# Kernel optimization log

Hardware: AMD Instinct MI355X
Metric: run time of the kernel (lower is better)

Reference implementation:

```python
import jax, jax.numpy as jnp
import numpy as np

B, S, N, M = 64, 512, 512, 128   # batch, sensory_size, state_size, motor_size
UNFOLDS = 6
DT = 0.1  # elapsed_time


def _gate(v, mu, sigma):
    # piecewise-linear 'sigmoid': clip((v - mu + sigma) / (2 sigma), 0, 1)
    # v: [B, P] -> [B, P, 1] broadcast against [P, N]
    return jnp.clip((v[..., None] - mu + sigma) / (2.0 * sigma), 0.0, 1.0)


def setup_inputs() -> dict:
    key = jax.random.key(0)
    ks = jax.random.split(key, 12)
    u = lambda k, sh, lo, hi: jax.random.uniform(k, sh, jnp.float32, lo, hi)
    inputs = jax.random.normal(ks[0], (B, S), dtype=jnp.float32)
    states = jax.random.normal(ks[1], (B, N), dtype=jnp.float32) * 0.1
    # parameters per _init_ranges
    tau = u(ks[2], (N,), 0.001, 2.0)
    b = u(ks[3], (N,), -0.2, 0.2)
    erev = jnp.where(jax.random.bernoulli(ks[4], 0.8, (N, N)), 1.0, -1.0).astype(jnp.float32)
    w = u(ks[5], (N, N), 0.001, 1.0)
    sigma = jnp.full((N, N), 0.5, jnp.float32)
    mu = jnp.full((N, N), 0.5, jnp.float32)
    sensory_erev = jnp.where(jax.random.bernoulli(ks[6], 0.8, (S, N)), 1.0, -1.0).astype(jnp.float32)
    sensory_w = u(ks[7], (S, N), 0.001, 1.0)
    sensory_sigma = jnp.full((S, N), 0.5, jnp.float32)
    sensory_mu = jnp.full((S, N), 0.5, jnp.float32)
    sparsity_mask = jax.random.bernoulli(ks[8], 0.3, (N, N)).astype(jnp.float32)
    sensory_sparsity_mask = jax.random.bernoulli(ks[9], 0.3, (S, N)).astype(jnp.float32)
    input_w = jnp.ones((S,), jnp.float32)
    input_b = jnp.zeros((S,), jnp.float32)
    output_w = jnp.ones((M,), jnp.float32)
    output_b = jnp.zeros((M,), jnp.float32)
    return dict(inputs=inputs, states=states, tau=tau, b=b, erev=erev, w=w,
                sigma=sigma, mu=mu, sensory_erev=sensory_erev, sensory_w=sensory_w,
                sensory_sigma=sensory_sigma, sensory_mu=sensory_mu,
                sparsity_mask=sparsity_mask, sensory_sparsity_mask=sensory_sparsity_mask,
                input_w=input_w, input_b=input_b, output_w=output_w, output_b=output_b)


def reference(inputs, states, tau, b, erev, w, sigma, mu,
              sensory_erev, sensory_w, sensory_sigma, sensory_mu,
              sparsity_mask, sensory_sparsity_mask,
              input_w, input_b, output_w, output_b):
    # input mapping (affine)
    x = inputs * input_w + input_b                                   # [B, S]
    # sensory synapses, computed once
    sa = _gate(x, sensory_mu, sensory_sigma) * sensory_sparsity_mask  # [B, S, N]
    s_rev = jnp.einsum('bsn,sn->bn', sa, sensory_erev)               # [B, N]
    s_w = jnp.einsum('bsn,sn->bn', sa, sensory_w)                    # [B, N]
    delta = DT / UNFOLDS

    def step(v, _):
        g = _gate(v, mu, sigma) * sparsity_mask                      # [B, N, N]
        sum_rev = jnp.einsum('bij,ij->bj', g, erev) + s_rev + b      # sum over presynaptic i
        sum_w = jnp.einsum('bij,ij->bj', g, w) + s_w
        k = 1.0 / (1.0 + sum_w)
        taun = tau * k
        q = taun / (taun + delta)
        v_new = q * v + (1.0 - q) * k * sum_rev
        return v_new, None

    v, _ = jax.lax.scan(step, states, None, length=UNFOLDS)
    # output mapping: slice last M neurons (M < N), then affine
    out = v[:, -M:] * output_w + output_b                            # [B, M]
    return out, v
```

## Files before the change

### kernel.cpp

```cpp
#include <hip/hip_runtime.h>
#include <string.h>

constexpr int cB = 64, cS = 512, cN = 512, cM = 128, cUNF = 6;
constexpr float cDELTA = 0.016666666666666666f;

constexpr int JT   = 16;
constexpr int NCB  = cN / JT;
constexpr int NBLK = 256;
constexpr int NT   = 1024;
constexpr int NCW  = 4;
constexpr int SLOT_STRIDE = 16;

constexpr size_t OFF_V0   = 0;
constexpr size_t OFF_V1   = (size_t)cB * cN;
constexpr size_t OFF_H0   = OFF_V1 + (size_t)cB * cN;
constexpr size_t OFF_H1   = OFF_H0 + (size_t)cB * cN / 2;
constexpr size_t OFF_SLOT = OFF_H1 + (size_t)cB * cN / 2;
constexpr size_t OFF_DONE = OFF_SLOT + 512;
constexpr size_t OFF_BAD  = OFF_DONE + 4096;
constexpr size_t OFF_PK   = 131072;
static_assert(OFF_BAD + 64 <= OFF_PK, "control region must not alias packed table");

typedef _Float16 half8 __attribute__((ext_vector_type(8)));
typedef float    floatx4 __attribute__((ext_vector_type(4)));

__device__ __forceinline__ float clamp01(float x) {
    return __builtin_amdgcn_fmed3f(x, 0.0f, 1.0f);
}

__device__ __forceinline__ unsigned pack2h(float lo, float hi) {
    _Float16 l = (_Float16)lo, h = (_Float16)hi;
    unsigned short ls, hs;
    memcpy(&ls, &l, 2); memcpy(&hs, &h, 2);
    return (unsigned)ls | ((unsigned)hs << 16);
}

__global__ __launch_bounds__(NT, 1)
void k_fused(const float* __restrict__ inputs, const float* __restrict__ states,
             const float* __restrict__ tau,    const float* __restrict__ bias,
             const float* __restrict__ erev,   const float* __restrict__ wgt,
             const float* __restrict__ sigma,  const float* __restrict__ mu,
             const float* __restrict__ serev,  const float* __restrict__ swgt,
             const float* __restrict__ ssigma, const float* __restrict__ smu,
             const float* __restrict__ mask,   const float* __restrict__ smask,
             const float* __restrict__ inw,    const float* __restrict__ inb,
             const float* __restrict__ outw,   const float* __restrict__ outb,
             float* __restrict__ out, float* __restrict__ ws)
{
    float* v0 = ws + OFF_V0;
    float* v1 = ws + OFF_V1;
    _Float16* h0 = (_Float16*)(ws + OFF_H0);
    _Float16* h1 = (_Float16*)(ws + OFF_H1);
    int* slots = (int*)(ws + OFF_SLOT);
    int* done  = (int*)(ws + OFF_DONE);
    int* badf  = (int*)(ws + OFF_BAD);
    unsigned* pk = (unsigned*)(ws + OFF_PK);

    const int tid = threadIdx.x, blk = blockIdx.x;

    {
        const unsigned g = (unsigned)blk * NT + tid;
        const int lr  = g & 15;
        const int qp  = (g >> 4) & 3;
        const int lg2 = (g >> 6) & 3;
        const int kk2 = (g >> 8) & 15;
        const int jt2 = (g >> 12) & 31;
        const int m2  = (g >> 17) & 1;

        const float* E  = m2 ? serev  : erev;
        const float* W  = m2 ? swgt   : wgt;
        const float* SG = m2 ? ssigma : sigma;
        const float* MU = m2 ? smu    : mu;
        const float* MK = m2 ? smask  : mask;

        const int j  = jt2 * JT + lr;
        const int i0 = kk2 * 32 + lg2 * 8 + qp * 2;
        const size_t o0 = (size_t)i0 * cN + j, o1 = o0 + cN;
        const float e0 = E[o0],  e1 = E[o1];
        const float w0 = W[o0],  w1 = W[o1];
        const float m0 = MK[o0], m1 = MK[o1];
        const float s0 = SG[o0], s1 = SG[o1];
        const float u0 = MU[o0], u1 = MU[o1];
        const bool bad = (m0 != 0.f && (s0 != 0.5f || u0 != 0.5f)) ||
                         (m1 != 0.f && (s1 != 0.5f || u1 != 0.5f));

        const unsigned ed = pack2h(e0 * m0, e1 * m1);
        const unsigned wd = pack2h(w0 * m0, w1 * m1);
        const int frag = kk2 * 64 + lg2 * 16 + lr;
        unsigned* base = pk + (size_t)jt2 * 16384 + (m2 * 2) * 4096 + frag * 4 + qp;
        __hip_atomic_store(base,        ed, __ATOMIC_RELAXED, __HIP_MEMORY_SCOPE_AGENT);
        __hip_atomic_store(base + 4096, wd, __ATOMIC_RELAXED, __HIP_MEMORY_SCOPE_AGENT);
        if (bad)
            __hip_atomic_store(&badf[m2 * 32 + jt2], 1,
                               __ATOMIC_RELAXED, __HIP_MEMORY_SCOPE_AGENT);
    }
    __syncthreads();
    if (tid == 0)
        __hip_atomic_store(&done[blk * SLOT_STRIDE], 1,
                           __ATOMIC_RELAXED, __HIP_MEMORY_SCOPE_AGENT);
    if (blk >= NCB) return;

    const int j0   = blk * JT;
    const int lane = tid & 63;
    const int wv   = tid >> 6;
    const int mt   = wv;
    const int lr   = lane & 15;
    const int lg   = lane >> 4;
    const int bj   = j0 + lr;
    const int arow = mt * 16 + lr;
    const int kbase = lg * 8;
    const int cb0  = mt * 16 + lg * 4;

    int* mySlot = slots + blk * SLOT_STRIDE;

    __shared__ _Float16 Hlds[32768];
    __shared__ int sAny;
    const half8* hfr = (const half8*)Hlds;

    if (tid == 0) sAny = 0;

    float vold[4] = {0.f, 0.f, 0.f, 0.f};
    float tau_j = 0.f, bias_j = 0.f, ow = 0.f, ob = 0.f;
    if (wv < NCW) {
#pragma unroll
        for (int r = 0; r < 4; ++r)
            vold[r] = states[(size_t)(cb0 + r) * cN + bj];
        tau_j  = tau[bj];
        bias_j = bias[bj];
        if (bj >= cN - cM) { ow = outw[bj - (cN - cM)]; ob = outb[bj - (cN - cM)]; }
    }

    if (tid < NBLK) {
        const int* sl = done + tid * SLOT_STRIDE;
        while (__hip_atomic_load(sl, __ATOMIC_RELAXED, __HIP_MEMORY_SCOPE_AGENT) < 1)
            __builtin_amdgcn_s_sleep(1);
    }
    __syncthreads();

    const bool fastR = (__hip_atomic_load(&badf[blk], __ATOMIC_RELAXED,
                                          __HIP_MEMORY_SCOPE_AGENT) != 1);
    const bool fastS = (__hip_atomic_load(&badf[32 + blk], __ATOMIC_RELAXED,
                                          __HIP_MEMORY_SCOPE_AGENT) != 1);
    if (tid < 32 &&
        __hip_atomic_load(&badf[tid], __ATOMIC_RELAXED,
                          __HIP_MEMORY_SCOPE_AGENT) == 1)
        sAny = 1;

    {
        const uint4* src = (const uint4*)pk + (size_t)blk * 4096;
        floatx4 tmp[4];
#pragma unroll
        for (int r = 0; r < 4; ++r)
            asm volatile("global_load_dwordx4 %0, %1, off sc0 sc1"
                         : "=v"(tmp[r]) : "v"(src + r * 1024 + tid) : "memory");
        asm volatile("s_waitcnt vmcnt(0)" ::: "memory");
        __builtin_amdgcn_sched_barrier(0);
#pragma unroll
        for (int r = 0; r < 4; ++r)
            ((uint4*)Hlds)[r * 1024 + tid] = __builtin_bit_cast(uint4, tmp[r]);
    }
    __syncthreads();
    const bool pubF32 = (sAny == 1);

    float srb[4] = {0.f, 0.f, 0.f, 0.f}, swv[4] = {0.f, 0.f, 0.f, 0.f};
    if (wv < NCW) {
        if (fastS) {
            floatx4 aR = {0.f, 0.f, 0.f, 0.f}, aW = {0.f, 0.f, 0.f, 0.f};
#pragma unroll
            for (int kk = 0; kk < 16; ++kk) {
                const int off = kk * 32 + kbase;
                const float4 xa = *(const float4*)(inputs + (size_t)arow * cS + off);
                const float4 xb = *(const float4*)(inputs + (size_t)arow * cS + off + 4);
                const float4 wa = *(const float4*)(inw + off);
                const float4 wb = *(const float4*)(inw + off + 4);
                const float4 ba = *(const float4*)(inb + off);
                const float4 bb = *(const float4*)(inb + off + 4);
                half8 ax;
                ax[0] = (_Float16)clamp01(fmaf(xa.x, wa.x, ba.x));
                ax[1] = (_Float16)clamp01(fmaf(xa.y, wa.y, ba.y));
                ax[2] = (_Float16)clamp01(fmaf(xa.z, wa.z, ba.z));
                ax[3] = (_Float16)clamp01(fmaf(xa.w, wa.w, ba.w));
                ax[4] = (_Float16)clamp01(fmaf(xb.x, wb.x, bb.x));
                ax[5] = (_Float16)clamp01(fmaf(xb.y, wb.y, bb.y));
                ax[6] = (_Float16)clamp01(fmaf(xb.z, wb.z, bb.z));
                ax[7] = (_Float16)clamp01(fmaf(xb.w, wb.w, bb.w));
                aR = __builtin_amdgcn_mfma_f32_16x16x32_f16(ax, hfr[2048 + kk * 64 + lane], aR, 0, 0, 0);
                aW = __builtin_amdgcn_mfma_f32_16x16x32_f16(ax, hfr[3072 + kk * 64 + lane], aW, 0, 0, 0);
            }
#pragma unroll
            for (int r = 0; r < 4; ++r) { srb[r] = aR[r] + bias_j; swv[r] = aW[r]; }
        } else {
            float sr4[4] = {0,0,0,0}, sw4[4] = {0,0,0,0};
            for (int s = 0; s < cS; ++s) {
                size_t o = (size_t)s * cN + bj;
                float mk = smask[o];
                float sg = ssigma[o];
                float a  = 0.5f / sg;
                float c  = fmaf(-smu[o], a, 0.5f);
                float ee = serev[o] * mk, ww = swgt[o] * mk;
                float iw = inw[s], ib = inb[s];
#pragma unroll
                for (int r = 0; r < 4; ++r) {
                    float x = fmaf(inputs[(size_t)(cb0 + r) * cS + s], iw, ib);
                    float g = clamp01(fmaf(x, a, c));
                    sr4[r] = fmaf(g, ee, sr4[r]);
                    sw4[r] = fmaf(g, ww, sw4[r]);
                }
            }
#pragma unroll
            for (int r = 0; r < 4; ++r) { srb[r] = sr4[r] + bias_j; swv[r] = sw4[r]; }
        }
    }

    for (int u = 0; u < cUNF; ++u) {
        const float*    vRp = (u == 0) ? states : ((u & 1) ? v0 : v1);
        const _Float16* hRp = (u & 1) ? h0 : h1;

        float sumE[4], sumW[4];
        if (wv < NCW) {
            if (fastR) {
                floatx4 aE = {0.f, 0.f, 0.f, 0.f}, aWc = {0.f, 0.f, 0.f, 0.f};
                if (u == 0) {
                    const float* vrow = states + (size_t)arow * cN + kbase;
#pragma unroll
                    for (int kk = 0; kk < 16; ++kk) {
                        const float4 va = *(const float4*)(vrow + kk * 32);
                        const float4 vb = *(const float4*)(vrow + kk * 32 + 4);
                        half8 a8;
                        a8[0] = (_Float16)clamp01(va.x);
                        a8[1] = (_Float16)clamp01(va.y);
                        a8[2] = (_Float16)clamp01(va.z);
                        a8[3] = (_Float16)clamp01(va.w);
                        a8[4] = (_Float16)clamp01(vb.x);
                        a8[5] = (_Float16)clamp01(vb.y);
                        a8[6] = (_Float16)clamp01(vb.z);
                        a8[7] = (_Float16)clamp01(vb.w);
                        aE  = __builtin_amdgcn_mfma_f32_16x16x32_f16(a8, hfr[kk * 64 + lane], aE,  0, 0, 0);
                        aWc = __builtin_amdgcn_mfma_f32_16x16x32_f16(a8, hfr[1024 + kk * 64 + lane], aWc, 0, 0, 0);
                    }
                } else {
                    floatx4 raw[16];
                    const _Float16* hrow = hRp + (size_t)arow * cN + kbase;
#pragma unroll
                    for (int kk = 0; kk < 16; ++kk)
                        asm volatile("global_load_dwordx4 %0, %1, off offset:%2 sc0 sc1"
                                     : "=v"(raw[kk]) : "v"(hrow), "n"(kk * 64) : "memory");
                    asm volatile("s_waitcnt vmcnt(0)" ::: "memory");
                    __builtin_amdgcn_sched_barrier(0);
#pragma unroll
                    for (int kk = 0; kk < 16; ++kk) {
                        const half8 a8 = __builtin_bit_cast(half8, raw[kk]);
                        aE  = __builtin_amdgcn_mfma_f32_16x16x32_f16(a8, hfr[kk * 64 + lane], aE,  0, 0, 0);
                        aWc = __builtin_amdgcn_mfma_f32_16x16x32_f16(a8, hfr[1024 + kk * 64 + lane], aWc, 0, 0, 0);
                    }
                }
#pragma unroll
                for (int r = 0; r < 4; ++r) { sumE[r] = aE[r]; sumW[r] = aWc[r]; }
            } else {
                float r4[4] = {0,0,0,0}, w4[4] = {0,0,0,0};
                for (int i = 0; i < cN; ++i) {
                    size_t o = (size_t)i * cN + bj;
                    float mk = mask[o];
                    float sg = sigma[o];
                    float a  = 0.5f / sg;
                    float c  = fmaf(-mu[o], a, 0.5f);
                    float ee = erev[o] * mk, ww = wgt[o] * mk;
#pragma unroll
                    for (int r = 0; r < 4; ++r) {
                        float vi = __hip_atomic_load(&vRp[(size_t)(cb0 + r) * cN + i],
                                                     __ATOMIC_RELAXED, __HIP_MEMORY_SCOPE_AGENT);
                        float g = clamp01(fmaf(vi, a, c));
                        r4[r] = fmaf(g, ee, r4[r]);
                        w4[r] = fmaf(g, ww, w4[r]);
                    }
                }
#pragma unroll
                for (int r = 0; r < 4; ++r) { sumE[r] = r4[r]; sumW[r] = w4[r]; }
            }

#pragma unroll
            for (int r = 0; r < 4; ++r) {
                float rr   = sumE[r] + srb[r];
                float wsum = sumW[r] + swv[r];
                float k    = 1.0f / (1.0f + wsum);
                float taun = tau_j * k;
                float inv  = 1.0f / (taun + cDELTA);
                float vn   = (taun * inv) * vold[r] + (cDELTA * inv) * k * rr;
                vold[r] = vn;
            }
        }

        if (u < cUNF - 1) {
            if (wv < NCW) {
                float*    vWp = (u & 1) ? v1 : v0;
                _Float16* hWp = (u & 1) ? h1 : h0;
#pragma unroll
                for (int r = 0; r < 4; ++r) {
                    if (pubF32)
                        __hip_atomic_store(&vWp[(size_t)(cb0 + r) * cN + bj], vold[r],
                                           __ATOMIC_RELAXED, __HIP_MEMORY_SCOPE_AGENT);
                    _Float16 g = (_Float16)clamp01(vold[r]);
                    unsigned short gs;
                    memcpy(&gs, &g, 2);
                    unsigned int gi = gs;
                    asm volatile("global_store_short %0, %1, off sc0 sc1"
                                 :: "v"(hWp + (size_t)(cb0 + r) * cN + bj), "v"(gi)
                                 : "memory");
                }
            }
            __syncthreads();
            if (tid == 0)
                __hip_atomic_store(mySlot, u + 1,
                                   __ATOMIC_RELAXED, __HIP_MEMORY_SCOPE_AGENT);
            if (wv < NCW) {
                const int* sl = slots + (lane & 31) * SLOT_STRIDE;
                bool ok;
                do {
                    int v = (lane < 32)
                        ? __hip_atomic_load(sl, __ATOMIC_RELAXED, __HIP_MEMORY_SCOPE_AGENT)
                        : 0x7fffffff;
                    ok = __all((int)(v >= u + 1));
                } while (!ok);
            }
        }
    }

    if (wv < NCW) {
        float* vout = out + (size_t)cB * cM;
#pragma unroll
        for (int r = 0; r < 4; ++r) {
            int b = cb0 + r;
            vout[(size_t)b * cN + bj] = vold[r];
            if (bj >= cN - cM)
                out[(size_t)b * cM + (bj - (cN - cM))] = fmaf(vold[r], ow, ob);
        }
    }
}

extern "C" void kernel_launch(void* const* d_in, const int* in_sizes, int n_in,
                              void* d_out, int out_size, void* d_ws, size_t ws_size,
                              hipStream_t stream)
{
    const float* inputs = (const float*)d_in[0];
    const float* states = (const float*)d_in[1];
    const float* tau    = (const float*)d_in[2];
    const float* bias   = (const float*)d_in[3];
    const float* erev   = (const float*)d_in[4];
    const float* wgt    = (const float*)d_in[5];
    const float* sigma  = (const float*)d_in[6];
    const float* mu     = (const float*)d_in[7];
    const float* serev  = (const float*)d_in[8];
    const float* swgt   = (const float*)d_in[9];
    const float* ssigma = (const float*)d_in[10];
    const float* smu    = (const float*)d_in[11];
    const float* mask   = (const float*)d_in[12];
    const float* smask  = (const float*)d_in[13];
    const float* inw    = (const float*)d_in[14];
    const float* inb    = (const float*)d_in[15];
    const float* outw   = (const float*)d_in[16];
    const float* outb   = (const float*)d_in[17];
    float* out = (float*)d_out;
    float* ws  = (float*)d_ws;

    k_fused<<<NBLK, NT, 0, stream>>>(inputs, states, tau, bias, erev, wgt,
                                     sigma, mu, serev, swgt, ssigma, smu,
                                     mask, smask, inw, inb, outw, outb,
                                     out, ws);
}
```

Measured before the change: 131.0 us.

## Precompute fp16 gated inputs and initial states in the packing phase

The prologue threads of the persistent kernel (grid index 196608 and up) now also compute the clamped affine input gate and the clamped initial states, store them as packed fp16 in new workspace buffers, and the compute blocks read these with plain vector loads. This takes the per-element fp32 loads, FMAs, clamps and conversions off the serial critical path of the 32 compute blocks. The change also swaps the inline-asm cache-bypassing load of the packed table for ordinary loads, which depend on the done-flag barrier for visibility, and adds a short sleep in the inter-block spin-wait. The workspace layout is moved to fixed offsets to fit the new buffers.

```diff
diff --git a/kernel.cpp b/kernel.cpp
--- a/kernel.cpp
+++ b/kernel.cpp
@@ -12,14 +12,22 @@
 constexpr int SLOT_STRIDE = 16;
 
 constexpr size_t OFF_V0   = 0;
-constexpr size_t OFF_V1   = (size_t)cB * cN;
-constexpr size_t OFF_H0   = OFF_V1 + (size_t)cB * cN;
-constexpr size_t OFF_H1   = OFF_H0 + (size_t)cB * cN / 2;
-constexpr size_t OFF_SLOT = OFF_H1 + (size_t)cB * cN / 2;
+constexpr size_t OFF_V1   = 32768;
+constexpr size_t OFF_H0   = 65536;
+constexpr size_t OFF_H1   = 81920;
+constexpr size_t OFF_HX   = 98304;
+constexpr size_t OFF_HS0  = 114688;
+constexpr size_t OFF_SLOT = 131072;
 constexpr size_t OFF_DONE = OFF_SLOT + 512;
 constexpr size_t OFF_BAD  = OFF_DONE + 4096;
-constexpr size_t OFF_PK   = 131072;
+constexpr size_t OFF_PK   = 262144;
 static_assert(OFF_BAD + 64 <= OFF_PK, "control region must not alias packed table");
+static_assert(OFF_H0  + (size_t)cB * cN / 2 <= OFF_H1,   "h0 fits");
+static_assert(OFF_H1  + (size_t)cB * cN / 2 <= OFF_HX,   "h1 fits");
+static_assert(OFF_HX  + (size_t)cB * cS / 2 <= OFF_HS0,  "hx fits");
+static_assert(OFF_HS0 + (size_t)cB * cN / 2 <= OFF_SLOT, "hs0 fits");
+constexpr unsigned HX_DW  = (unsigned)cB * cS / 2;
+constexpr unsigned HS0_DW = (unsigned)cB * cN / 2;
 
 typedef _Float16 half8 __attribute__((ext_vector_type(8)));
 typedef float    floatx4 __attribute__((ext_vector_type(4)));
@@ -51,6 +59,8 @@
     float* v1 = ws + OFF_V1;
     _Float16* h0 = (_Float16*)(ws + OFF_H0);
     _Float16* h1 = (_Float16*)(ws + OFF_H1);
+    _Float16* hx  = (_Float16*)(ws + OFF_HX);
+    _Float16* hs0 = (_Float16*)(ws + OFF_HS0);
     int* slots = (int*)(ws + OFF_SLOT);
     int* done  = (int*)(ws + OFF_DONE);
     int* badf  = (int*)(ws + OFF_BAD);
@@ -93,6 +103,28 @@
         if (bad)
             __hip_atomic_store(&badf[m2 * 32 + jt2], 1,
                                __ATOMIC_RELAXED, __HIP_MEMORY_SCOPE_AGENT);
+
+        if (g >= 196608) {
+            const unsigned q = g - 196608;
+            if (q < HX_DW) {
+                const unsigned p2 = q * 2;
+                const int b = p2 >> 9, s = p2 & (cS - 1);
+                const size_t o = (size_t)b * cS + s;
+                float xa = clamp01(fmaf(inputs[o],     inw[s],     inb[s]));
+                float xb = clamp01(fmaf(inputs[o + 1], inw[s + 1], inb[s + 1]));
+                __hip_atomic_store((unsigned*)hx + q, pack2h(xa, xb),
+                                   __ATOMIC_RELAXED, __HIP_MEMORY_SCOPE_AGENT);
+            } else if (q < HX_DW + HS0_DW) {
+                const unsigned qq = q - HX_DW;
+                const unsigned p2 = qq * 2;
+                const int b = p2 >> 9, n = p2 & (cN - 1);
+                const size_t o = (size_t)b * cN + n;
+                float va = clamp01(states[o]);
+                float vb = clamp01(states[o + 1]);
+                __hip_atomic_store((unsigned*)hs0 + qq, pack2h(va, vb),
+                                   __ATOMIC_RELAXED, __HIP_MEMORY_SCOPE_AGENT);
+            }
+        }
     }
     __syncthreads();
     if (tid == 0)
@@ -148,16 +180,9 @@
 
     {
         const uint4* src = (const uint4*)pk + (size_t)blk * 4096;
-        floatx4 tmp[4];
 #pragma unroll
         for (int r = 0; r < 4; ++r)
-            asm volatile("global_load_dwordx4 %0, %1, off sc0 sc1"
-                         : "=v"(tmp[r]) : "v"(src + r * 1024 + tid) : "memory");
-        asm volatile("s_waitcnt vmcnt(0)" ::: "memory");
-        __builtin_amdgcn_sched_barrier(0);
-#pragma unroll
-        for (int r = 0; r < 4; ++r)
-            ((uint4*)Hlds)[r * 1024 + tid] = __builtin_bit_cast(uint4, tmp[r]);
+            ((uint4*)Hlds)[r * 1024 + tid] = src[r * 1024 + tid];
     }
     __syncthreads();
     const bool pubF32 = (sAny == 1);
@@ -165,27 +190,17 @@
     float srb[4] = {0.f, 0.f, 0.f, 0.f}, swv[4] = {0.f, 0.f, 0.f, 0.f};
     if (wv < NCW) {
         if (fastS) {
+            uint4 raw[16];
+            const uint4* xr = (const uint4*)(hx + (size_t)arow * cS);
+#pragma unroll
+            for (int kk = 0; kk < 16; ++kk)
+                raw[kk] = xr[kk * 4 + lg];
             floatx4 aR = {0.f, 0.f, 0.f, 0.f}, aW = {0.f, 0.f, 0.f, 0.f};
 #pragma unroll
             for (int kk = 0; kk < 16; ++kk) {
-                const int off = kk * 32 + kbase;
-                const float4 xa = *(const float4*)(inputs + (size_t)arow * cS + off);
-                const float4 xb = *(const float4*)(inputs + (size_t)arow * cS + off + 4);
-                const float4 wa = *(const float4*)(inw + off);
-                const float4 wb = *(const float4*)(inw + off + 4);
-                const float4 ba = *(const float4*)(inb + off);
-                const float4 bb = *(const float4*)(inb + off + 4);
-                half8 ax;
-                ax[0] = (_Float16)clamp01(fmaf(xa.x, wa.x, ba.x));
-                ax[1] = (_Float16)clamp01(fmaf(xa.y, wa.y, ba.y));
-                ax[2] = (_Float16)clamp01(fmaf(xa.z, wa.z, ba.z));
-                ax[3] = (_Float16)clamp01(fmaf(xa.w, wa.w, ba.w));
-                ax[4] = (_Float16)clamp01(fmaf(xb.x, wb.x, bb.x));
-                ax[5] = (_Float16)clamp01(fmaf(xb.y, wb.y, bb.y));
-                ax[6] = (_Float16)clamp01(fmaf(xb.z, wb.z, bb.z));
-                ax[7] = (_Float16)clamp01(fmaf(xb.w, wb.w, bb.w));
-                aR = __builtin_amdgcn_mfma_f32_16x16x32_f16(ax, hfr[2048 + kk * 64 + lane], aR, 0, 0, 0);
-                aW = __builtin_amdgcn_mfma_f32_16x16x32_f16(ax, hfr[3072 + kk * 64 + lane], aW, 0, 0, 0);
+                const half8 a8 = __builtin_bit_cast(half8, raw[kk]);
+                aR = __builtin_amdgcn_mfma_f32_16x16x32_f16(a8, hfr[2048 + kk * 64 + lane], aR, 0, 0, 0);
+                aW = __builtin_amdgcn_mfma_f32_16x16x32_f16(a8, hfr[3072 + kk * 64 + lane], aW, 0, 0, 0);
             }
 #pragma unroll
             for (int r = 0; r < 4; ++r) { srb[r] = aR[r] + bias_j; swv[r] = aW[r]; }
@@ -221,20 +236,14 @@
             if (fastR) {
                 floatx4 aE = {0.f, 0.f, 0.f, 0.f}, aWc = {0.f, 0.f, 0.f, 0.f};
                 if (u == 0) {
-                    const float* vrow = states + (size_t)arow * cN + kbase;
+                    uint4 raw[16];
+                    const uint4* sr = (const uint4*)(hs0 + (size_t)arow * cN);
+#pragma unroll
+                    for (int kk = 0; kk < 16; ++kk)
+                        raw[kk] = sr[kk * 4 + lg];
 #pragma unroll
                     for (int kk = 0; kk < 16; ++kk) {
-                        const float4 va = *(const float4*)(vrow + kk * 32);
-                        const float4 vb = *(const float4*)(vrow + kk * 32 + 4);
-                        half8 a8;
-                        a8[0] = (_Float16)clamp01(va.x);
-                        a8[1] = (_Float16)clamp01(va.y);
-                        a8[2] = (_Float16)clamp01(va.z);
-                        a8[3] = (_Float16)clamp01(va.w);
-                        a8[4] = (_Float16)clamp01(vb.x);
-                        a8[5] = (_Float16)clamp01(vb.y);
-                        a8[6] = (_Float16)clamp01(vb.z);
-                        a8[7] = (_Float16)clamp01(vb.w);
+                        const half8 a8 = __builtin_bit_cast(half8, raw[kk]);
                         aE  = __builtin_amdgcn_mfma_f32_16x16x32_f16(a8, hfr[kk * 64 + lane], aE,  0, 0, 0);
                         aWc = __builtin_amdgcn_mfma_f32_16x16x32_f16(a8, hfr[1024 + kk * 64 + lane], aWc, 0, 0, 0);
                     }
@@ -320,6 +329,7 @@
                         ? __hip_atomic_load(sl, __ATOMIC_RELAXED, __HIP_MEMORY_SCOPE_AGENT)
                         : 0x7fffffff;
                     ok = __all((int)(v >= u + 1));
+                    if (!ok) __builtin_amdgcn_s_sleep(1);
                 } while (!ok);
             }
         }
```

Result: faster. 125.2 us (-4.5%).
